# Performance work log

Measured on AMD Instinct MI355X. Metric: run time of the kernel, lower is better.

The kernel has to match this reference:

```python
import jax, jax.numpy as jnp
import numpy as np

POOLSCALE = 4  # HSA: avg-pool kernel/stride = (scale, scale*4)

def _avg_pool(x, kh, kw):
    # kernel == stride and dims divisible -> exact reshape-mean pooling
    B, C, H, W = x.shape
    return x.reshape(B, C, H // kh, kh, W // kw, kw).mean(axis=(3, 5))

def setup_inputs() -> dict:
    key = jax.random.key(0)
    k1, k2, k3 = jax.random.split(key, 3)
    shape = (4, 64, 192, 192)
    return {
        "K": jax.random.normal(k1, shape, dtype=jnp.float32),
        "Q": jax.random.normal(k2, shape, dtype=jnp.float32),
        "V": jax.random.normal(k3, shape, dtype=jnp.float32),
    }

def reference(K, Q, V):
    B, C, H, W = Q.shape
    kh, kw = POOLSCALE, POOLSCALE * 4
    Qp = Q.reshape(B, C, H * W).transpose(0, 2, 1)          # [B, HW, C]
    Kp = _avg_pool(K, kh, kw)                               # [B, C, h, w]
    Kp = Kp.reshape(B, C, -1)                               # [B, C, hw_p]
    Vp = _avg_pool(V, kh, kw).reshape(B, C, -1)             # [B, C, hw_p]
    scores = jnp.einsum('bnc,bcm->bnm', Qp, Kp)             # [B, HW, hw_p]
    attn = jax.nn.softmax(scores, axis=1)                   # softmax over query dim (dim=1), as in torch code
    out = jnp.einsum('bcm,bnm->bcn', Vp, attn)              # V_pie @ attn^T -> [B, C, HW]
    return out.reshape(B, C, H, W)
```

## Files before the change

kernel.cpp:

```cpp
#include <hip/hip_runtime.h>
#include <stdint.h>

#define BB 4
#define CC 64
#define HH 192
#define WW 192
#define HWN (HH*WW)
#define KH 4
#define KW 16
#define PW (WW/KW)
#define MP ((HH/KH)*(WW/KW))
#define MITER (MP/64)
#define SCALE_W 65536.0f
#define INV_SCALE (1.0f/65536.0f)

typedef _Float16 half8 __attribute__((ext_vector_type(8)));
typedef _Float16 half4 __attribute__((ext_vector_type(4)));
typedef float floatx4 __attribute__((ext_vector_type(4)));

static __device__ __forceinline__ void gload16(const void* g, void* l) {
  __builtin_amdgcn_global_load_lds((const __attribute__((address_space(1))) void*)g,
                                   (__attribute__((address_space(3))) void*)l, 16, 0, 0);
}
#define WAITCNT_VM(N) asm volatile("s_waitcnt vmcnt(" #N ")" ::: "memory")
#define WAITCNT_LGKM0 asm volatile("s_waitcnt lgkmcnt(0)" ::: "memory")


__global__ __launch_bounds__(256) void pool_kernel(
    const float* __restrict__ Kin, const float* __restrict__ Vin,
    _Float16* __restrict__ kptF, float* __restrict__ vp) {
  int t = blockIdx.x * 256 + threadIdx.x;
  const int total = BB * CC * MP;
  bool isV = t >= total;
  int idx = isV ? t - total : t;
  int m = idx % MP;
  int c = (idx / MP) % CC;
  int b = idx / (MP * CC);
  int mh = m / PW, mw = m % PW;
  const float* src = (isV ? Vin : Kin) + (((b * CC + c) * HH + mh * KH) * WW + mw * KW);
  float s = 0.f;
#pragma unroll
  for (int r = 0; r < KH; ++r) {
    const float4* row = (const float4*)(src + r * WW);
#pragma unroll
    for (int j = 0; j < KW / 4; ++j) {
      float4 v = row[j];
      s += v.x + v.y + v.z + v.w;
    }
  }
  s *= (1.0f / (KH * KW));
  if (isV) {
    vp[(b * CC + c) * MP + m] = s;
  } else {
    int mi = m >> 6, mloc = m & 63, l15 = mloc >> 2, mf = mloc & 3;
    int ks = c >> 5, lhi = (c >> 3) & 3, e = c & 7;
    int lane = lhi * 16 + l15;
    kptF[(((((b * MITER + mi) * 4 + mf) * 2 + ks)) * 64 + lane) * 8 + e] = (_Float16)s;
  }
}

__global__ __launch_bounds__(512) void colsum_kernel(
    const float* __restrict__ Q, const _Float16* __restrict__ kptF,
    float* __restrict__ colsum) {
  __shared__ float cs[MP];
  __shared__ char stg[MITER * 8 * 1024];
  int b = blockIdx.y;
  int n0 = blockIdx.x * 256;
  int tid = threadIdx.x;
  int wv = tid >> 6;
  int lane = tid & 63;
  int l15 = lane & 15, lhi = lane >> 4;

  for (int i = tid; i < MP; i += 512) cs[i] = 0.f;

  const _Float16* kb = kptF + b * MITER * 8 * 512;
#pragma unroll
  for (int j = 0; j < 9; ++j) {
    int q = wv * 9 + j;
    gload16(kb + q * 512 + lane * 8, stg + q * 1024);
  }

  const float* Qb = Q + b * CC * HWN;
  int nrow = n0 + wv * 32 + l15;
  half8 afrag[2][2];
#pragma unroll
  for (int nf = 0; nf < 2; ++nf)
#pragma unroll
    for (int ks = 0; ks < 2; ++ks)
#pragma unroll
      for (int e = 0; e < 8; ++e)
        afrag[nf][ks][e] = (_Float16)Qb[(ks * 32 + lhi * 8 + e) * HWN + nrow + nf * 16];

  __syncthreads();

  floatx4 zero = {0.f, 0.f, 0.f, 0.f};
#pragma unroll
  for (int mi = 0; mi < MITER; ++mi) {
    half8 bfr[4][2];
#pragma unroll
    for (int mf = 0; mf < 4; ++mf)
#pragma unroll
      for (int ks = 0; ks < 2; ++ks)
        bfr[mf][ks] = *(const half8*)(stg + ((mi * 4 + mf) * 2 + ks) * 1024 + lane * 16);
    floatx4 sacc[2][4];
#pragma unroll
    for (int nf = 0; nf < 2; ++nf)
#pragma unroll
      for (int mf = 0; mf < 4; ++mf) sacc[nf][mf] = zero;
    __builtin_amdgcn_s_setprio(1);
#pragma unroll
    for (int ks = 0; ks < 2; ++ks)
#pragma unroll
      for (int nf = 0; nf < 2; ++nf)
#pragma unroll
        for (int mf = 0; mf < 4; ++mf)
          sacc[nf][mf] = __builtin_amdgcn_mfma_f32_16x16x32_f16(
              afrag[nf][ks], bfr[mf][ks], sacc[nf][mf], 0, 0, 0);
    __builtin_amdgcn_s_setprio(0);
#pragma unroll
    for (int mf = 0; mf < 4; ++mf) {
      float s = 0.f;
#pragma unroll
      for (int nf = 0; nf < 2; ++nf)
#pragma unroll
        for (int r = 0; r < 4; ++r)
          s += __expf(sacc[nf][mf][r]);
      s += __shfl_xor(s, 16);
      s += __shfl_xor(s, 32);
      if (lane < 16) atomicAdd(&cs[mi * 64 + l15 * 4 + mf], s);
    }
  }
  __syncthreads();
  for (int i = tid; i < MP; i += 512) atomicAdd(&colsum[b * MP + i], cs[i]);
}

__global__ __launch_bounds__(256) void wprep_kernel(
    const float* __restrict__ vp, const float* __restrict__ colsum,
    _Float16* __restrict__ wqF) {
  int t = blockIdx.x * 256 + threadIdx.x;
  int m = t % MP;
  int c = (t / MP) % CC;
  int b = t / (CC * MP);
  float w = vp[t] / colsum[b * MP + m] * SCALE_W;
  int cf = c >> 4, l15 = c & 15;
  int mi = m >> 6, mloc = m & 63;
  int ks = mloc >> 5, lhi = (mloc >> 3) & 3, e = mloc & 7;
  int lane = lhi * 16 + l15;
  wqF[((((b * MITER + mi) * 4 + cf) * 2 + ks) * 64 + lane) * 8 + e] = (_Float16)w;
}

__global__ __launch_bounds__(256) void attn_main_kernel(
    const float* __restrict__ Q, const _Float16* __restrict__ kptF,
    const _Float16* __restrict__ wqF, float* __restrict__ out) {
  __shared__ char lds[3 * 16384 + 4 * 4096];
  char* stg = lds;
  int b = blockIdx.y;
  int n0 = blockIdx.x * 128;
  int tid = threadIdx.x;
  int wv = tid >> 6;
  int lane = tid & 63;
  int l15 = lane & 15, lhi = lane >> 4;
  char* eb = lds + 49152 + wv * 4096;

  const _Float16* kb = kptF + b * MITER * 8 * 512;
  const _Float16* wb = wqF + b * MITER * 8 * 512;

#define STAGE_A(tt, ss)                                                        \
  {                                                                            \
    int q0_ = wv * 4;                                                          \
    _Pragma("unroll") for (int j_ = 0; j_ < 4; ++j_) {                         \
      int q_ = q0_ + j_;                                                       \
      const _Float16* sp_ = (q_ < 8 ? kb + (tt) * 4096 + q_ * 512              \
                                    : wb + (tt) * 4096 + (q_ - 8) * 512) +     \
                            lane * 8;                                          \
      gload16(sp_, stg + (ss) * 16384 + q_ * 1024);                            \
    }                                                                          \
  }

  STAGE_A(0, 0);
  STAGE_A(1, 1);

  const float* Qb = Q + b * CC * HWN;
  int nrow = n0 + wv * 32 + l15;
  half8 afrag[2][2];
#pragma unroll
  for (int nf = 0; nf < 2; ++nf)
#pragma unroll
    for (int ks = 0; ks < 2; ++ks)
#pragma unroll
      for (int e = 0; e < 8; ++e)
        afrag[nf][ks][e] = (_Float16)Qb[(ks * 32 + lhi * 8 + e) * HWN + nrow + nf * 16];

  floatx4 zero = {0.f, 0.f, 0.f, 0.f};
  floatx4 oacc[4][2];
#pragma unroll
  for (int cf = 0; cf < 4; ++cf)
#pragma unroll
    for (int nf = 0; nf < 2; ++nf) oacc[cf][nf] = zero;

  WAITCNT_VM(4);
  __builtin_amdgcn_sched_barrier(0);
  __builtin_amdgcn_s_barrier();

#pragma unroll
  for (int mi = 0; mi < MITER; ++mi) {
    const int sc = mi % 3;
    const int spv = (mi + 2) % 3;

    if (mi >= 1) {
      if (mi <= 7) { WAITCNT_VM(4); } else { WAITCNT_VM(0); }
      __builtin_amdgcn_sched_barrier(0);
      __builtin_amdgcn_s_barrier();
    }

    half8 bfr[4][2];
#pragma unroll
    for (int mf = 0; mf < 4; ++mf)
#pragma unroll
      for (int ks = 0; ks < 2; ++ks)
        bfr[mf][ks] = *(const half8*)(stg + sc * 16384 + (mf * 2 + ks) * 1024 + lane * 16);
    half8 wfr[4][2];
    half8 ef[2][2];
    if (mi >= 1) {
#pragma unroll
      for (int cf = 0; cf < 4; ++cf)
#pragma unroll
        for (int ks = 0; ks < 2; ++ks)
          wfr[cf][ks] = *(const half8*)(stg + spv * 16384 + 8192 + (cf * 2 + ks) * 1024 + lane * 16);
#pragma unroll
      for (int nf = 0; nf < 2; ++nf)
#pragma unroll
        for (int ks = 0; ks < 2; ++ks) {
          int nl = nf * 16 + l15;
          int slot = (ks * 4 + lhi) ^ (nl & 7);
          ef[nf][ks] = *(const half8*)(eb + nl * 128 + (slot << 4));
        }
    }

    WAITCNT_LGKM0;
    __builtin_amdgcn_sched_barrier(0);
    __builtin_amdgcn_s_barrier();

    if (mi + 2 < MITER) STAGE_A(mi + 2, spv);

    floatx4 sacc[2][4];
#pragma unroll
    for (int nf = 0; nf < 2; ++nf)
#pragma unroll
      for (int mf = 0; mf < 4; ++mf) sacc[nf][mf] = zero;
    __builtin_amdgcn_s_setprio(1);
#pragma unroll
    for (int ks = 0; ks < 2; ++ks)
#pragma unroll
      for (int nf = 0; nf < 2; ++nf)
#pragma unroll
        for (int mf = 0; mf < 4; ++mf)
          sacc[nf][mf] = __builtin_amdgcn_mfma_f32_16x16x32_f16(
              afrag[nf][ks], bfr[mf][ks], sacc[nf][mf], 0, 0, 0);
    if (mi >= 1) {
#pragma unroll
      for (int ks = 0; ks < 2; ++ks)
#pragma unroll
        for (int cf = 0; cf < 4; ++cf)
#pragma unroll
          for (int nf = 0; nf < 2; ++nf)
            oacc[cf][nf] = __builtin_amdgcn_mfma_f32_16x16x32_f16(
                wfr[cf][ks], ef[nf][ks], oacc[cf][nf], 0, 0, 0);
    }
    __builtin_amdgcn_s_setprio(0);

#pragma unroll
    for (int nf = 0; nf < 2; ++nf)
#pragma unroll
      for (int r = 0; r < 4; ++r) {
        int nl = nf * 16 + lhi * 4 + r;
        half4 h;
#pragma unroll
        for (int mf = 0; mf < 4; ++mf) h[mf] = (_Float16)__expf(sacc[nf][mf][r]);
        int byte = nl * 128 + ((((l15 >> 1) ^ (nl & 7))) << 4) + ((l15 & 1) << 3);
        *(half4*)(eb + byte) = h;
      }
  }

  {
    half8 wfr[4][2];
#pragma unroll
    for (int cf = 0; cf < 4; ++cf)
#pragma unroll
      for (int ks = 0; ks < 2; ++ks)
        wfr[cf][ks] = *(const half8*)(stg + 2 * 16384 + 8192 + (cf * 2 + ks) * 1024 + lane * 16);
    half8 ef[2][2];
#pragma unroll
    for (int nf = 0; nf < 2; ++nf)
#pragma unroll
      for (int ks = 0; ks < 2; ++ks) {
        int nl = nf * 16 + l15;
        int slot = (ks * 4 + lhi) ^ (nl & 7);
        ef[nf][ks] = *(const half8*)(eb + nl * 128 + (slot << 4));
      }
    __builtin_amdgcn_s_setprio(1);
#pragma unroll
    for (int ks = 0; ks < 2; ++ks)
#pragma unroll
      for (int cf = 0; cf < 4; ++cf)
#pragma unroll
        for (int nf = 0; nf < 2; ++nf)
          oacc[cf][nf] = __builtin_amdgcn_mfma_f32_16x16x32_f16(
              wfr[cf][ks], ef[nf][ks], oacc[cf][nf], 0, 0, 0);
    __builtin_amdgcn_s_setprio(0);
  }

  float* ob = out + b * CC * HWN;
#pragma unroll
  for (int cf = 0; cf < 4; ++cf)
#pragma unroll
    for (int nf = 0; nf < 2; ++nf)
#pragma unroll
      for (int r = 0; r < 4; ++r) {
        int c = cf * 16 + lhi * 4 + r;
        int n = n0 + wv * 32 + nf * 16 + l15;
        ob[c * HWN + n] = oacc[cf][nf][r] * INV_SCALE;
      }
}

extern "C" void kernel_launch(void* const* d_in, const int* in_sizes, int n_in,
                              void* d_out, int out_size, void* d_ws, size_t ws_size,
                              hipStream_t stream) {
  const float* K = (const float*)d_in[0];
  const float* Q = (const float*)d_in[1];
  const float* V = (const float*)d_in[2];
  float* out = (float*)d_out;
  char* ws = (char*)d_ws;
  _Float16* kptF  = (_Float16*)(ws);
  float*    vp    = (float*)(ws + 294912);
  _Float16* wqF   = (_Float16*)(ws + 294912 + 589824);
  float*    colsum = (float*)(ws + 294912 + 589824 + 294912);

  hipMemsetAsync(colsum, 0, BB * MP * sizeof(float), stream);
  pool_kernel<<<(2 * BB * CC * MP) / 256, 256, 0, stream>>>(K, V, kptF, vp);
  colsum_kernel<<<dim3(HWN / 256, BB), 512, 0, stream>>>(Q, kptF, colsum);
  wprep_kernel<<<(BB * CC * MP) / 256, 256, 0, stream>>>(vp, colsum, wqF);
  attn_main_kernel<<<dim3(HWN / 128, BB), 256, 0, stream>>>(Q, kptF, wqF, out);
}
```

Baseline: 97.94 us.

## Split colsum by key tile per wave, write partials, add reduce kernel

```diff
diff --git a/kernel.cpp b/kernel.cpp
--- a/kernel.cpp
+++ b/kernel.cpp
@@ -11,6 +11,7 @@
 #define PW (WW/KW)
 #define MP ((HH/KH)*(WW/KW))
 #define MITER (MP/64)
+#define NCHUNK (HWN/256)
 #define SCALE_W 65536.0f
 #define INV_SCALE (1.0f/65536.0f)
 
@@ -59,49 +60,40 @@
   }
 }
 
-__global__ __launch_bounds__(512) void colsum_kernel(
+__global__ __launch_bounds__(576) void colsum_kernel(
     const float* __restrict__ Q, const _Float16* __restrict__ kptF,
-    float* __restrict__ colsum) {
-  __shared__ float cs[MP];
-  __shared__ char stg[MITER * 8 * 1024];
+    float* __restrict__ part) {
   int b = blockIdx.y;
   int n0 = blockIdx.x * 256;
   int tid = threadIdx.x;
-  int wv = tid >> 6;
+  int wv = tid / 64;
   int lane = tid & 63;
   int l15 = lane & 15, lhi = lane >> 4;
 
-  for (int i = tid; i < MP; i += 512) cs[i] = 0.f;
-
   const _Float16* kb = kptF + b * MITER * 8 * 512;
-#pragma unroll
-  for (int j = 0; j < 9; ++j) {
-    int q = wv * 9 + j;
-    gload16(kb + q * 512 + lane * 8, stg + q * 1024);
-  }
+  half8 bfr[4][2];
+#pragma unroll
+  for (int mf = 0; mf < 4; ++mf)
+#pragma unroll
+    for (int ks = 0; ks < 2; ++ks)
+      bfr[mf][ks] = *(const half8*)(kb + ((wv * 4 + mf) * 2 + ks) * 512 + lane * 8);
 
   const float* Qb = Q + b * CC * HWN;
-  int nrow = n0 + wv * 32 + l15;
-  half8 afrag[2][2];
-#pragma unroll
-  for (int nf = 0; nf < 2; ++nf)
-#pragma unroll
-    for (int ks = 0; ks < 2; ++ks)
-#pragma unroll
-      for (int e = 0; e < 8; ++e)
-        afrag[nf][ks][e] = (_Float16)Qb[(ks * 32 + lhi * 8 + e) * HWN + nrow + nf * 16];
-
-  __syncthreads();
-
   floatx4 zero = {0.f, 0.f, 0.f, 0.f};
-#pragma unroll
-  for (int mi = 0; mi < MITER; ++mi) {
-    half8 bfr[4][2];
-#pragma unroll
-    for (int mf = 0; mf < 4; ++mf)
+  float s0 = 0.f, s1 = 0.f, s2 = 0.f, s3 = 0.f;
+
+#pragma unroll
+  for (int it = 0; it < 8; ++it) {
+    int nr = n0 + it * 32 + l15;
+    half8 af[2][2];
+#pragma unroll
+    for (int nf = 0; nf < 2; ++nf)
 #pragma unroll
       for (int ks = 0; ks < 2; ++ks)
-        bfr[mf][ks] = *(const half8*)(stg + ((mi * 4 + mf) * 2 + ks) * 1024 + lane * 16);
+#pragma unroll
+        for (int e = 0; e < 8; ++e)
+          af[nf][ks][e] = (_Float16)Qb[(ks * 32 + lhi * 8 + e) * HWN + nr + nf * 16];
+
     floatx4 sacc[2][4];
 #pragma unroll
     for (int nf = 0; nf < 2; ++nf)
@@ -115,23 +107,45 @@
 #pragma unroll
         for (int mf = 0; mf < 4; ++mf)
           sacc[nf][mf] = __builtin_amdgcn_mfma_f32_16x16x32_f16(
-              afrag[nf][ks], bfr[mf][ks], sacc[nf][mf], 0, 0, 0);
+              af[nf][ks], bfr[mf][ks], sacc[nf][mf], 0, 0, 0);
     __builtin_amdgcn_s_setprio(0);
-#pragma unroll
-    for (int mf = 0; mf < 4; ++mf) {
-      float s = 0.f;
-#pragma unroll
-      for (int nf = 0; nf < 2; ++nf)
-#pragma unroll
-        for (int r = 0; r < 4; ++r)
-          s += __expf(sacc[nf][mf][r]);
-      s += __shfl_xor(s, 16);
-      s += __shfl_xor(s, 32);
-      if (lane < 16) atomicAdd(&cs[mi * 64 + l15 * 4 + mf], s);
-    }
-  }
-  __syncthreads();
-  for (int i = tid; i < MP; i += 512) atomicAdd(&colsum[b * MP + i], cs[i]);
+
+#pragma unroll
+    for (int nf = 0; nf < 2; ++nf)
+#pragma unroll
+      for (int r = 0; r < 4; ++r) {
+        s0 += __expf(sacc[nf][0][r]);
+        s1 += __expf(sacc[nf][1][r]);
+        s2 += __expf(sacc[nf][2][r]);
+        s3 += __expf(sacc[nf][3][r]);
+      }
+  }
+
+  s0 += __shfl_xor(s0, 16); s0 += __shfl_xor(s0, 32);
+  s1 += __shfl_xor(s1, 16); s1 += __shfl_xor(s1, 32);
+  s2 += __shfl_xor(s2, 16); s2 += __shfl_xor(s2, 32);
+  s3 += __shfl_xor(s3, 16); s3 += __shfl_xor(s3, 32);
+  if (lane < 16) {
+    float* p = part + (b * NCHUNK + blockIdx.x) * MP + wv * 64 + l15 * 4;
+    p[0] = s0; p[1] = s1; p[2] = s2; p[3] = s3;
+  }
+}
+
+__global__ __launch_bounds__(256) void colsum_reduce_kernel(
+    const float* __restrict__ part, float* __restrict__ colsum) {
+  int t = blockIdx.x * 256 + threadIdx.x;
+  int m = t % MP;
+  int b = t / MP;
+  const float* p = part + b * NCHUNK * MP + m;
+  float a0 = 0.f, a1 = 0.f, a2 = 0.f, a3 = 0.f;
+#pragma unroll 4
+  for (int nc = 0; nc < NCHUNK; nc += 4) {
+    a0 += p[(nc + 0) * MP];
+    a1 += p[(nc + 1) * MP];
+    a2 += p[(nc + 2) * MP];
+    a3 += p[(nc + 3) * MP];
+  }
+  colsum[t] = (a0 + a1) + (a2 + a3);
 }
 
 __global__ __launch_bounds__(256) void wprep_kernel(
@@ -149,7 +163,7 @@
   wqF[((((b * MITER + mi) * 4 + cf) * 2 + ks) * 64 + lane) * 8 + e] = (_Float16)w;
 }
 
-__global__ __launch_bounds__(256) void attn_main_kernel(
+__global__ __launch_bounds__(256, 2) void attn_main_kernel(
     const float* __restrict__ Q, const _Float16* __restrict__ kptF,
     const _Float16* __restrict__ wqF, float* __restrict__ out) {
   __shared__ char lds[3 * 16384 + 4 * 4096];
@@ -335,10 +349,11 @@
   float*    vp    = (float*)(ws + 294912);
   _Float16* wqF   = (_Float16*)(ws + 294912 + 589824);
   float*    colsum = (float*)(ws + 294912 + 589824 + 294912);
-
-  hipMemsetAsync(colsum, 0, BB * MP * sizeof(float), stream);
+  float*    part  = out;
+
   pool_kernel<<<(2 * BB * CC * MP) / 256, 256, 0, stream>>>(K, V, kptF, vp);
-  colsum_kernel<<<dim3(HWN / 256, BB), 512, 0, stream>>>(Q, kptF, colsum);
+  colsum_kernel<<<dim3(NCHUNK, BB), 576, 0, stream>>>(Q, kptF, part);
+  colsum_reduce_kernel<<<(BB * MP) / 256, 256, 0, stream>>>(part, colsum);
   wprep_kernel<<<(BB * CC * MP) / 256, 256, 0, stream>>>(vp, colsum, wqF);
   attn_main_kernel<<<dim3(HWN / 128, BB), 256, 0, stream>>>(Q, kptF, wqF, out);
 }
```

Result: no change. 99.23 us (+1.3%).
